# Kernel optimization log

Measured on AMD Instinct MI355X. Metric: run time of the kernel, lower is better.

Reference implementation:

```python
import jax, jax.numpy as jnp
import numpy as np

B, NV, H, W = 4, 1, 224, 224
GH = GW = 16                 # 224 // 14 patch grid
NT = 1 + GH * GW             # 257 tokens (cls + patches)
CIN, DF, DH = 1152, 512, 128
NP0 = 512
UPF = (4, 8)
RADIUS = 1.0


def setup_inputs():
    key = jax.random.key(0)
    ks = jax.random.split(key, 8)
    rn = lambda k, s, sc: jax.random.normal(k, s) * sc
    points = jax.random.uniform(ks[0], (B, NP0, 3), minval=-0.5, maxval=0.5)
    tokens = rn(ks[1], (B, CIN, NT), 0.5)
    # OpenGL-style c2w (the forward flips cols 1:3 to OpenCV); camera at z=+2 looking at origin
    c2w = np.tile(np.eye(4, dtype=np.float32), (B, NV, 1, 1))
    c2w[..., 2, 3] = 2.0
    K = np.zeros((B, NV, 3, 3), dtype=np.float32)
    K[..., 0, 0] = 250.0; K[..., 1, 1] = 250.0
    K[..., 0, 2] = W / 2.0; K[..., 1, 2] = H / 2.0
    K[..., 2, 2] = 1.0
    return dict(
        points=points, input_image_tokens=tokens,
        c2w_cond=jnp.asarray(c2w), intrinsic_cond=jnp.asarray(K),
        w1=rn(ks[2], (2 * DF, CIN), CIN ** -0.5), b1=jnp.zeros((2 * DF,)),
        w2=rn(ks[3], (DF, 2 * DF), (2 * DF) ** -0.5), b2=jnp.zeros((DF,)),
        s0_w1=rn(ks[4], (DH, 3 + DF), (3 + DF) ** -0.5), s0_b1=jnp.zeros((DH,)),
        s0_ow=rn(ks[5], (UPF[0] * 3, DH), DH ** -0.5), s0_ob=jnp.zeros((UPF[0] * 3,)),
        s1_w1=rn(ks[6], (DH, 3 + DF), (3 + DF) ** -0.5), s1_b1=jnp.zeros((DH,)),
        s1_ow=rn(ks[7], (UPF[1] * 3, DH), DH ** -0.5), s1_ob=jnp.zeros((UPF[1] * 3,)))


def _points_projection(pts, c2w, K, lf):
    # pts: (B,N,3), c2w: (B,4,4) OpenCV, K: (B,3,3), lf: (B,C,H,W)
    N = pts.shape[1]
    w2c = jnp.linalg.inv(c2w)
    cam = jnp.einsum('bij,bnj->bni', w2c[:, :3, :3], pts) + w2c[:, None, :3, 3]
    z = cam[..., 2]
    zs = jnp.where(jnp.abs(z) > 1e-8, z, 1e-8)
    px = K[:, 0, 0][:, None] * cam[..., 0] / zs + K[:, 0, 2][:, None]
    py = K[:, 1, 1][:, None] * cam[..., 1] / zs + K[:, 1, 2][:, None]
    ix = jnp.floor(px).astype(jnp.int32)
    iy = jnp.floor(py).astype(jnp.int32)
    valid = (z > 1e-6) & (ix >= 0) & (ix < W) & (iy >= 0) & (iy < H)
    pix = jnp.where(valid, iy * W + ix, H * W)                  # (B,N); dummy bin H*W
    nseg = B * (H * W + 1)
    seg = (jnp.arange(B)[:, None] * (H * W + 1) + pix).reshape(-1)
    zf = jnp.where(valid, z, jnp.inf).reshape(-1)
    minz = jax.ops.segment_min(zf, seg, num_segments=nseg)      # z-buffer (points_per_pixel=1)
    ismin = valid.reshape(-1) & (zf <= minz[seg])
    pid = jnp.arange(B * N)
    win = jax.ops.segment_min(jnp.where(ismin, pid, B * N), seg, num_segments=nseg)
    visible = (pid == win[seg]).reshape(B, N)                   # unique winner per pixel
    lff = lf.reshape(B, -1, H * W)
    g = jnp.take_along_axis(lff, jnp.clip(pix, 0, H * W - 1)[:, None, :], axis=2)  # (B,C,N)
    return jnp.where(visible[:, None, :], g, 0.0)


def reference(points, input_image_tokens, c2w_cond, intrinsic_cond,
              w1, b1, w2, b2, s0_w1, s0_b1, s0_ow, s0_ob, s1_w1, s1_b1, s1_ow, s1_ob):
    # mlp_feat_cond: 1x1 conv MLP over tokens
    feat = jax.nn.relu(jnp.einsum('oc,bcn->bon', w1, input_image_tokens) + b1[:, None])
    feat = jnp.einsum('oc,bcn->bon', w2, feat) + b2[:, None]    # (B, DF, NT)
    # OpenGL -> OpenCV flip of c2w columns 1:3
    flip = jnp.ones((4, 4)).at[:3, 1:3].set(-1.0)
    c2w = c2w_cond[:, 0] * flip
    Kmat = intrinsic_cond[:, 0]
    # drop cls token, to patch grid, bilinear upsample to image resolution
    lf = jnp.transpose(feat, (0, 2, 1))[:, 1:].reshape(B, GH, GW, DF)
    lf = jnp.transpose(lf, (0, 3, 1, 2))
    lf = jax.image.resize(lf, (B, DF, H, W), method='bilinear')  # (B, DF, H, W)
    pts = points
    pcd = jnp.transpose(points, (0, 2, 1))                      # (B,3,N)
    stages = (((s0_w1, s0_b1, s0_ow, s0_ob), UPF[0]), ((s1_w1, s1_b1, s1_ow, s1_ob), UPF[1]))
    outs = []
    for (ws, bs, ow, ob), f in stages:
        up_cond = _points_projection(pts, c2w, Kmat, lf)        # (B, DF, N) visibility-masked gather
        h = jax.nn.relu(jnp.einsum('oc,bcn->bon', ws,
                                   jnp.concatenate([pcd, up_cond], axis=1)) + bs[:, None])
        off = jnp.tanh(jnp.einsum('oc,bcn->bon', ow, h) + ob[:, None])  # (B, 3f, N)
        n = pcd.shape[2]
        off = off.reshape(B, f, 3, n).transpose(0, 2, 3, 1).reshape(B, 3, n * f)
        pcd = jnp.repeat(pcd, f, axis=2) + off * RADIUS         # SPD-style bounded upsample
        pts = jnp.transpose(pcd, (0, 2, 1))
        outs.append(pts)
    return tuple(outs)
```

## Files before the change

kernel.cpp:

```cpp
#include <hip/hip_runtime.h>
#include <hip/hip_bf16.h>
#include <cstdint>
#include <cstddef>

using bf16 = __hip_bfloat16;
typedef __attribute__((ext_vector_type(8))) short bf16x8_t;
typedef __attribute__((ext_vector_type(4))) float f32x4_t;

#define BB 4
#define HH 224
#define WWD 224
#define NTOK 257
#define CINC 1152
#define DFC 512

constexpr size_t OFF_WC     = 256;
constexpr size_t OFF_T      = OFF_WC + 1052672;
constexpr size_t OFF_FP     = OFF_T + 1048576;
constexpr size_t OFF_ZB0    = OFF_FP + 12582912;
constexpr size_t OFF_ZB1    = OFF_ZB0 + 1605632;
constexpr size_t OFF_PI0    = OFF_ZB1 + 1605632;
constexpr size_t OFF_PI1    = OFF_PI0 + 32768;
constexpr size_t WS_FULL4   = OFF_PI1 + 131072;
constexpr size_t OFF_SCR    = 256 + 2105344;
constexpr size_t OFF_ZBUF   = OFF_SCR;
constexpr size_t OFF_PINFO  = OFF_SCR + 1605632;
constexpr size_t WS_NEED    = OFF_SCR + 1736704;

__device__ __forceinline__ float ldf(const void* p, size_t i, bool f32) {
  return f32 ? ((const float*)p)[i] : __bfloat162float(((const bf16*)p)[i]);
}
__device__ __forceinline__ double ldd(const void* p, size_t i, bool f32) {
  return f32 ? (double)((const float*)p)[i]
             : (double)__bfloat162float(((const bf16*)p)[i]);
}
__device__ __forceinline__ bool detect_f32(const void* c2w_raw) {
  const float* fc = (const float*)c2w_raw;
  return (fc[0] == 1.0f) && (fc[5] == 1.0f);
}

__device__ void compute_cam(const void* c2w_raw, const void* K_raw, int b, bool f32,
                            double* cw) {
  double m[16];
#pragma unroll
  for (int i = 0; i < 16; ++i) m[i] = ldd(c2w_raw, b*16 + i, f32);
  m[1]=-m[1]; m[2]=-m[2]; m[5]=-m[5]; m[6]=-m[6]; m[9]=-m[9]; m[10]=-m[10];
  double i0  =  m[5]*m[10]*m[15] - m[5]*m[11]*m[14] - m[9]*m[6]*m[15] + m[9]*m[7]*m[14] + m[13]*m[6]*m[11] - m[13]*m[7]*m[10];
  double i4  = -m[4]*m[10]*m[15] + m[4]*m[11]*m[14] + m[8]*m[6]*m[15] - m[8]*m[7]*m[14] - m[12]*m[6]*m[11] + m[12]*m[7]*m[10];
  double i8  =  m[4]*m[9]*m[15]  - m[4]*m[11]*m[13] - m[8]*m[5]*m[15] + m[8]*m[7]*m[13] + m[12]*m[5]*m[11] - m[12]*m[7]*m[9];
  double i12 = -m[4]*m[9]*m[14]  + m[4]*m[10]*m[13] + m[8]*m[5]*m[14] - m[8]*m[6]*m[13] - m[12]*m[5]*m[10] + m[12]*m[6]*m[9];
  double i1  = -m[1]*m[10]*m[15] + m[1]*m[11]*m[14] + m[9]*m[2]*m[15] - m[9]*m[3]*m[14] - m[13]*m[2]*m[11] + m[13]*m[3]*m[10];
  double i5  =  m[0]*m[10]*m[15] - m[0]*m[11]*m[14] - m[8]*m[2]*m[15] + m[8]*m[3]*m[14] + m[12]*m[2]*m[11] - m[12]*m[3]*m[10];
  double i9  = -m[0]*m[9]*m[15]  + m[0]*m[11]*m[13] + m[8]*m[1]*m[15] - m[8]*m[3]*m[13] - m[12]*m[1]*m[11] + m[12]*m[3]*m[9];
  double i13 =  m[0]*m[9]*m[14]  - m[0]*m[10]*m[13] - m[8]*m[1]*m[14] + m[8]*m[2]*m[13] + m[12]*m[1]*m[10] - m[12]*m[2]*m[9];
  double i2  =  m[1]*m[6]*m[15]  - m[1]*m[7]*m[14]  - m[5]*m[2]*m[15] + m[5]*m[3]*m[14] + m[13]*m[2]*m[7]  - m[13]*m[3]*m[6];
  double i6  = -m[0]*m[6]*m[15]  + m[0]*m[7]*m[14]  + m[4]*m[2]*m[15] - m[4]*m[3]*m[14] - m[12]*m[2]*m[7]  + m[12]*m[3]*m[6];
  double i10 =  m[0]*m[5]*m[15]  - m[0]*m[7]*m[13]  - m[4]*m[1]*m[15] + m[4]*m[3]*m[13] + m[12]*m[1]*m[7]  - m[12]*m[3]*m[5];
  double i14 = -m[0]*m[5]*m[14]  + m[0]*m[6]*m[13]  + m[4]*m[1]*m[14] - m[4]*m[2]*m[13] - m[12]*m[1]*m[6]  + m[12]*m[2]*m[5];
  double i3  = -m[1]*m[6]*m[11]  + m[1]*m[7]*m[10]  + m[5]*m[2]*m[11] - m[5]*m[3]*m[10] - m[9]*m[2]*m[7]   + m[9]*m[3]*m[6];
  double i7  =  m[0]*m[6]*m[11]  - m[0]*m[7]*m[10]  - m[4]*m[2]*m[11] + m[4]*m[3]*m[10] + m[8]*m[2]*m[7]   - m[8]*m[3]*m[6];
  double i11 = -m[0]*m[5]*m[11]  + m[0]*m[7]*m[9]   + m[4]*m[1]*m[11] - m[4]*m[3]*m[9]  - m[8]*m[1]*m[7]   + m[8]*m[3]*m[5];
  double det = m[0]*i0 + m[1]*i4 + m[2]*i8 + m[3]*i12;
  double r = 1.0 / det;
  cw[0]=i0*r;  cw[1]=i1*r;  cw[2]=i2*r;  cw[3]=i3*r;
  cw[4]=i4*r;  cw[5]=i5*r;  cw[6]=i6*r;  cw[7]=i7*r;
  cw[8]=i8*r;  cw[9]=i9*r;  cw[10]=i10*r; cw[11]=i11*r;
  cw[12] = ldd(K_raw, b*9+0, f32);
  cw[13] = ldd(K_raw, b*9+2, f32);
  cw[14] = ldd(K_raw, b*9+4, f32);
  cw[15] = ldd(K_raw, b*9+5, f32);
}

__device__ __forceinline__ void project_point(
    double px, double py, double pz, const double* cw, int b, int m,
    unsigned long long* __restrict__ zbuf, int* __restrict__ pinfo) {
  double cx = cw[0]*px + cw[1]*py + cw[2]*pz + cw[3];
  double cy = cw[4]*px + cw[5]*py + cw[6]*pz + cw[7];
  double z  = cw[8]*px + cw[9]*py + cw[10]*pz + cw[11];
  double zs = (fabs(z) > 1e-8) ? z : 1e-8;
  double fpx = cw[12] * cx / zs + cw[13];
  double fpy = cw[14] * cy / zs + cw[15];
  double fix = floor(fpx), fiy = floor(fpy);
  bool valid = (z > 1e-6) && (fix >= 0.0) && (fix < (double)WWD) && (fiy >= 0.0) && (fiy < (double)HH);
  int* pi = pinfo + (size_t)m * 4;
  if (valid) {
    int ix = (int)fix, iy = (int)fiy;
    int zidx = b * (HH * WWD) + iy * WWD + ix;
    float zf = (float)z;
    unsigned long long key = ((unsigned long long)__float_as_uint(zf) << 32) | (unsigned)m;
    atomicMin(&zbuf[zidx], key);
    pi[0] = zidx; pi[1] = 1;
    *(unsigned long long*)(pi + 2) = key;
  } else {
    pi[0] = 0; pi[1] = 0; pi[2] = 0; pi[3] = 0;
  }
}

__global__ __launch_bounds__(256) void init_k(uint4* __restrict__ wcT,
                                              uint4* __restrict__ zb) {
  const int NW = 2101248 / 16;
  const int NZ = 3211264 / 16;
  int i = (int)blockIdx.x * 256 + (int)threadIdx.x;
  if (i < NW) {
    wcT[i] = make_uint4(0u, 0u, 0u, 0u);
  } else {
    int j = i - NW;
    if (j < NZ) zb[j] = make_uint4(~0u, ~0u, ~0u, ~0u);
  }
}

template <int XK, int WK, bool ATOMIC, bool PART, int PREC>
__device__ void gemm_body(
    short* SMEM, int bX, int bY, int bZ,
    const void* __restrict__ Wm, const void* __restrict__ Wm2,
    const void* __restrict__ X, const void* __restrict__ xb,
    int bstr, float* __restrict__ Y, const void* __restrict__ c2w_raw,
    int O, int K, int Nn, int Yld, int Xld, int Xc0,
    int bx0, int bxm, int by0, int bym,
    int Wld, int Wc0, int skn) {
  short* Whi = SMEM;
  short* Wmd = SMEM + 2560;
  short* Wlo = SMEM + 5120;
  short* Xhi = SMEM + 7680;
  short* Xmd = SMEM + 10240;
  short* Xlo = SMEM + 12800;
  const bool f32 = detect_f32(c2w_raw);
  int tid = threadIdx.x;
  int n0 = bX * 64;
  int o0 = bY * 64;
  int bidx = bZ / skn;
  int ks = bZ - bidx * skn;
  int bx = bx0 + bxm * bidx;
  int by = by0 + bym * bidx;
  int kq = K / skn;
  int kbase = ks * kq;
  int so  = tid >> 2;
  int skq = tid & 3;
  int sn  = tid & 63;
  int skg = tid >> 6;
  int wv = tid >> 6, lane = tid & 63;
  int lm = lane & 15, lq = lane >> 4;

  float wreg[8], xreg[8];
  f32x4_t acc[4] = {};

  auto load_w = [&](int c0) {
    if constexpr (WK == 3) {
      int orow = o0 + so;
      const void* Wp = (orow < 128) ? Wm : Wm2;
      size_t base = (size_t)(orow & 127) * Wld + Wc0 + c0 + skq * 8;
#pragma unroll
      for (int j = 0; j < 8; ++j) wreg[j] = ldf(Wp, base + j, f32);
    } else {
      size_t base = (size_t)(o0 + so) * Wld + c0 + skq * 8;
      if (f32) {
        const float* Wf = (const float*)Wm;
        float4 v0 = *(const float4*)(Wf + base);
        float4 v1 = *(const float4*)(Wf + base + 4);
        wreg[0]=v0.x; wreg[1]=v0.y; wreg[2]=v0.z; wreg[3]=v0.w;
        wreg[4]=v1.x; wreg[5]=v1.y; wreg[6]=v1.z; wreg[7]=v1.w;
      } else {
        const unsigned short* Wh = (const unsigned short*)Wm;
        ushort4 u0 = *(const ushort4*)(Wh + base);
        ushort4 u1 = *(const ushort4*)(Wh + base + 4);
        wreg[0]=__uint_as_float((unsigned)u0.x<<16); wreg[1]=__uint_as_float((unsigned)u0.y<<16);
        wreg[2]=__uint_as_float((unsigned)u0.z<<16); wreg[3]=__uint_as_float((unsigned)u0.w<<16);
        wreg[4]=__uint_as_float((unsigned)u1.x<<16); wreg[5]=__uint_as_float((unsigned)u1.y<<16);
        wreg[6]=__uint_as_float((unsigned)u1.z<<16); wreg[7]=__uint_as_float((unsigned)u1.w<<16);
      }
    }
  };
  auto load_x = [&](int c0) {
    int gn = n0 + sn;
#pragma unroll
    for (int j = 0; j < 8; ++j) {
      int c = c0 + skg * 8 + j;
      float v = 0.f;
      if (gn < Nn) {
        if (XK == 3) {
          v = (gn < 1024) ? ldf(X, (size_t)c * 1024 + gn, f32)
                          : ((gn == 1024) ? ldf(xb, c, f32) : 0.f);
        } else {
          size_t xi = ((size_t)bx * K + c) * Xld + Xc0 + gn;
          v = ldf(X, xi, f32);
        }
      }
      xreg[j] = v;
    }
  };
  auto store_hi = [&](const float* r, short* hp, int off) {
    int hd[4];
#pragma unroll
    for (int d = 0; d < 4; ++d) {
      unsigned b0 = __float_as_uint(r[2*d]), b1 = __float_as_uint(r[2*d+1]);
      hd[d] = (int)((b0 >> 16) | (b1 & 0xFFFF0000u));
    }
    *(int4*)&hp[off] = make_int4(hd[0], hd[1], hd[2], hd[3]);
  };
  auto split_store3 = [&](const float* r, short* hp, short* mp, short* lp, int off) {
    int hd[4], md[4], ld[4];
#pragma unroll
    for (int d = 0; d < 4; ++d) {
      float v0 = r[2*d], v1 = r[2*d+1];
      unsigned b0 = __float_as_uint(v0), b1 = __float_as_uint(v1);
      hd[d] = (int)((b0 >> 16) | (b1 & 0xFFFF0000u));
      float h0 = __uint_as_float(b0 & 0xFFFF0000u);
      float h1 = __uint_as_float(b1 & 0xFFFF0000u);
      float r0 = v0 - h0, r1 = v1 - h1;
      unsigned c0 = __float_as_uint(r0), c1 = __float_as_uint(r1);
      md[d] = (int)((c0 >> 16) | (c1 & 0xFFFF0000u));
      float m0 = __uint_as_float(c0 & 0xFFFF0000u);
      float m1 = __uint_as_float(c1 & 0xFFFF0000u);
      unsigned e0 = __float_as_uint(r0 - m0), e1 = __float_as_uint(r1 - m1);
      ld[d] = (int)((e0 >> 16) | (e1 & 0xFFFF0000u));
    }
    *(int4*)&hp[off] = make_int4(hd[0], hd[1], hd[2], hd[3]);
    *(int4*)&mp[off] = make_int4(md[0], md[1], md[2], md[3]);
    *(int4*)&lp[off] = make_int4(ld[0], ld[1], ld[2], ld[3]);
  };

  int nkt = kq / 32;
  int woff = so * 40 + skq * 8;
  int xoff = sn * 40 + skg * 8;
  int aoff = (wv * 16 + lm) * 40 + lq * 8;
  load_w(kbase); load_x(kbase);

  if (PREC == 0 && !f32) {
    for (int kt = 0; kt < nkt; ++kt) {
      __syncthreads();
      store_hi(wreg, Whi, woff);
      store_hi(xreg, Xhi, xoff);
      __syncthreads();
      if (kt + 1 < nkt) { load_w(kbase + (kt + 1) * 32); load_x(kbase + (kt + 1) * 32); }
      bf16x8_t ahi = *(const bf16x8_t*)&Whi[aoff];
#pragma unroll
      for (int nt = 0; nt < 4; ++nt) {
        int boff = (nt * 16 + lm) * 40 + lq * 8;
        bf16x8_t bhi = *(const bf16x8_t*)&Xhi[boff];
        acc[nt] = __builtin_amdgcn_mfma_f32_16x16x32_bf16(ahi, bhi, acc[nt], 0, 0, 0);
      }
    }
  } else {
    for (int kt = 0; kt < nkt; ++kt) {
      __syncthreads();
      split_store3(wreg, Whi, Wmd, Wlo, woff);
      split_store3(xreg, Xhi, Xmd, Xlo, xoff);
      __syncthreads();
      if (kt + 1 < nkt) { load_w(kbase + (kt + 1) * 32); load_x(kbase + (kt + 1) * 32); }
      bf16x8_t ahi = *(const bf16x8_t*)&Whi[aoff];
      bf16x8_t amd = *(const bf16x8_t*)&Wmd[aoff];
      bf16x8_t alo = *(const bf16x8_t*)&Wlo[aoff];
#pragma unroll
      for (int nt = 0; nt < 4; ++nt) {
        int boff = (nt * 16 + lm) * 40 + lq * 8;
        bf16x8_t bhi = *(const bf16x8_t*)&Xhi[boff];
        bf16x8_t bmd = *(const bf16x8_t*)&Xmd[boff];
        bf16x8_t blo = *(const bf16x8_t*)&Xlo[boff];
        acc[nt] = __builtin_amdgcn_mfma_f32_16x16x32_bf16(ahi, blo, acc[nt], 0, 0, 0);
        acc[nt] = __builtin_amdgcn_mfma_f32_16x16x32_bf16(amd, bmd, acc[nt], 0, 0, 0);
        acc[nt] = __builtin_amdgcn_mfma_f32_16x16x32_bf16(alo, bhi, acc[nt], 0, 0, 0);
        acc[nt] = __builtin_amdgcn_mfma_f32_16x16x32_bf16(amd, bhi, acc[nt], 0, 0, 0);
        acc[nt] = __builtin_amdgcn_mfma_f32_16x16x32_bf16(ahi, bmd, acc[nt], 0, 0, 0);
        acc[nt] = __builtin_amdgcn_mfma_f32_16x16x32_bf16(ahi, bhi, acc[nt], 0, 0, 0);
      }
    }
  }

  if constexpr (PART) {
    float* Yp = Y + (size_t)ks * (size_t)bstr;
#pragma unroll
    for (int nt = 0; nt < 4; ++nt) {
      int gn = n0 + nt * 16 + lm;
      if (gn < Nn) {
#pragma unroll
        for (int r = 0; r < 4; ++r) {
          int o = o0 + wv * 16 + lq * 4 + r;
          Yp[((size_t)by * O + o) * (size_t)Yld + gn] = acc[nt][r];
        }
      }
    }
  } else if (!ATOMIC) {
#pragma unroll
    for (int nt = 0; nt < 4; ++nt) {
      int gn = n0 + nt * 16 + lm;
      if (gn < Nn) {
#pragma unroll
        for (int r = 0; r < 4; ++r) {
          int o = o0 + wv * 16 + lq * 4 + r;
          Y[((size_t)by * O + o) * (size_t)Yld + gn] = acc[nt][r];
        }
      }
    }
  } else {
#pragma unroll
    for (int nt = 0; nt < 4; ++nt) {
      int gn = n0 + nt * 16 + lm;
      if (gn < Nn) {
#pragma unroll
        for (int r = 0; r < 4; ++r) {
          int o = o0 + wv * 16 + lq * 4 + r;
          atomicAdd(&Y[((size_t)by * O + o) * (size_t)Yld + gn], acc[nt][r]);
        }
      }
    }
  }
}

__global__ __launch_bounds__(256) void front_k(
    const void* __restrict__ w1, const void* __restrict__ tokens,
    float* __restrict__ fp,
    const void* __restrict__ s0w1, const void* __restrict__ s1w1,
    const void* __restrict__ w2, const void* __restrict__ b2,
    float* __restrict__ Wc, const void* __restrict__ c2w_raw) {
  __shared__ __align__(16) short SMEM[6 * 2560];
  int id = (int)blockIdx.x;
  if (id < 768) {
    gemm_body<0, 0, false, true, 0>(SMEM, id & 3, (id >> 2) & 15, id >> 6,
        w1, nullptr, tokens, nullptr,  1048576, fp, c2w_raw,
        1024, CINC, 256, 256, 257, 1, 0, 1, 0, 1, CINC, 0, 3);
  } else {
    int j = id - 768;
    gemm_body<3, 3, true, false, 0>(SMEM, j % 17, (j / 17) & 3, j / 68,
        s0w1, s1w1, w2, b2, 0, Wc, c2w_raw,
        256, 512, 1025, 1028, 1025, 0, 0, 0, 0, 0, 515, 3, 4);
  }
}

template <int SK>
__global__ __launch_bounds__(256) void tgemm_k(
    const float* __restrict__ Wc,
    const float* __restrict__ fp,
    const void* __restrict__ b1,
    float* __restrict__ T,
    const void* __restrict__ c2w_raw,
    const void* __restrict__ pts, const void* __restrict__ K_raw,
    unsigned long long* __restrict__ zb0, int* __restrict__ pinfo0) {
  const bool f32 = detect_f32(c2w_raw);
  if ((int)blockIdx.z == BB * SK) {
    int m = ((int)blockIdx.y * 4 + (int)blockIdx.x) * 256 + (int)threadIdx.x;
    if (m < BB * 512) {
      int b = m / 512;
      double cw[16];
      compute_cam(c2w_raw, K_raw, b, f32, cw);
      double px = ldd(pts, (size_t)m*3+0, f32);
      double py = ldd(pts, (size_t)m*3+1, f32);
      double pz = ldd(pts, (size_t)m*3+2, f32);
      project_point(px, py, pz, cw, b, m, zb0, pinfo0);
    }
    return;
  }
  const int TK = 32;
  const int PS = BB * 1024 * 256;
  __shared__ __align__(16) float uni[64 * 68];
  float* Ws = uni;
  float* Xs = uni + TK * 68;
  int tid = threadIdx.x;
  int n0 = blockIdx.x * 64;
  int o0 = blockIdx.y * 64;
  int bz = (int)blockIdx.z;
  int b  = bz / SK;
  int ks = bz - b * SK;
  const int kq = 1024 / SK;
  int kbase = ks * kq;
  int tx = tid & 15, ty = tid >> 4;
  int wo = tid >> 3, wk4 = tid & 7;
  float acc[4][4] = {};
  float4 wv[2];
  float xv[8];

  auto load_tile = [&](int c0) {
#pragma unroll
    for (int i = 0; i < 2; ++i) {
      int o = o0 + wo + i * 32;
      wv[i] = *(const float4*)(Wc + (size_t)o * 1028 + kbase + c0 + 4 * wk4);
    }
#pragma unroll
    for (int i = 0; i < 8; ++i) {
      int idx = i * 256 + tid;
      int n = idx & 63, k = idx >> 6;
      int kk = kbase + c0 + k;
      size_t xi = ((size_t)b * 1024 + kk) * 256 + n0 + n;
      float v = fp[xi] + fp[PS + xi] + fp[2 * PS + xi] + ldf(b1, kk, f32);
      xv[i] = fmaxf(v, 0.f);
    }
  };

  int nkt = kq / TK;
  load_tile(0);
  for (int kt = 0; kt < nkt; ++kt) {
    __syncthreads();
#pragma unroll
    for (int i = 0; i < 2; ++i) {
      int o = wo + i * 32;
      Ws[(4 * wk4 + 0) * 68 + o] = wv[i].x;
      Ws[(4 * wk4 + 1) * 68 + o] = wv[i].y;
      Ws[(4 * wk4 + 2) * 68 + o] = wv[i].z;
      Ws[(4 * wk4 + 3) * 68 + o] = wv[i].w;
    }
#pragma unroll
    for (int i = 0; i < 8; ++i) {
      int idx = i * 256 + tid;
      int n = idx & 63, k = idx >> 6;
      Xs[k * 68 + n] = xv[i];
    }
    __syncthreads();
    if (kt + 1 < nkt) load_tile((kt + 1) * TK);
#pragma unroll
    for (int k = 0; k < TK; ++k) {
      const float4 a  = *(const float4*)&Ws[k * 68 + tx * 4];
      const float4 bb = *(const float4*)&Xs[k * 68 + ty * 4];
      acc[0][0] = fmaf(a.x, bb.x, acc[0][0]); acc[0][1] = fmaf(a.x, bb.y, acc[0][1]);
      acc[0][2] = fmaf(a.x, bb.z, acc[0][2]); acc[0][3] = fmaf(a.x, bb.w, acc[0][3]);
      acc[1][0] = fmaf(a.y, bb.x, acc[1][0]); acc[1][1] = fmaf(a.y, bb.y, acc[1][1]);
      acc[1][2] = fmaf(a.y, bb.z, acc[1][2]); acc[1][3] = fmaf(a.y, bb.w, acc[1][3]);
      acc[2][0] = fmaf(a.z, bb.x, acc[2][0]); acc[2][1] = fmaf(a.z, bb.y, acc[2][1]);
      acc[2][2] = fmaf(a.z, bb.z, acc[2][2]); acc[2][3] = fmaf(a.z, bb.w, acc[2][3]);
      acc[3][0] = fmaf(a.w, bb.x, acc[3][0]); acc[3][1] = fmaf(a.w, bb.y, acc[3][1]);
      acc[3][2] = fmaf(a.w, bb.z, acc[3][2]); acc[3][3] = fmaf(a.w, bb.w, acc[3][3]);
    }
  }
  __syncthreads();
  float* ts = uni;
#pragma unroll
  for (int oi = 0; oi < 4; ++oi)
#pragma unroll
    for (int ni = 0; ni < 4; ++ni)
      ts[(tx * 4 + oi) * 65 + ty * 4 + ni] = acc[oi][ni];
  __syncthreads();
  int oo = tid & 63, nb = tid >> 6;
  float bv = (ks == 0) ? Wc[(size_t)(o0 + oo) * 1028 + 1024] : 0.f;
#pragma unroll
  for (int i = 0; i < 16; ++i) {
    int n = nb * 16 + i;
    atomicAdd(&T[((size_t)b * 256 + n0 + n) * 256 + o0 + oo], ts[oo * 65 + n] + bv);
  }
}

template <int XK, bool RELU, bool TROUT>
__global__ __launch_bounds__(256) void gemm_k(const void* __restrict__ Wm, const void* __restrict__ X,
                                              const void* __restrict__ bias, float* __restrict__ Y,
                                              const void* __restrict__ c2w_raw, int O, int K, int Nn,
                                              int bx0, int bxm, int by0, int bym) {
  const int TK = 32;
  __shared__ __align__(16) float Ws[TK * 68];
  __shared__ __align__(16) float Xs[TK * 68];
  const bool f32 = detect_f32(c2w_raw);
  int tid = threadIdx.x;
  int n0 = blockIdx.x * 64;
  int o0 = blockIdx.y * 64;
  int bx = bx0 + bxm * (int)blockIdx.z;
  int by = by0 + bym * (int)blockIdx.z;
  int tx = tid & 15, ty = tid >> 4;
  int wo  = tid >> 3;
  int wk4 = tid & 7;
  float acc[4][4] = {};
  float4 wv[2];
  float  xv[8];

  auto load_tile = [&](int c0) {
#pragma unroll
    for (int i = 0; i < 2; ++i) {
      int o = wo + i * 32;
      size_t off = (size_t)(o0 + o) * K + c0 + 4 * wk4;
      if (f32) {
        wv[i] = *(const float4*)((const float*)Wm + off);
      } else {
        ushort4 u = *(const ushort4*)((const unsigned short*)Wm + off);
        wv[i] = make_float4(__uint_as_float((unsigned)u.x << 16),
                            __uint_as_float((unsigned)u.y << 16),
                            __uint_as_float((unsigned)u.z << 16),
                            __uint_as_float((unsigned)u.w << 16));
      }
    }
#pragma unroll
    for (int i = 0; i < 8; ++i) {
      int idx = i * 256 + tid;
      int n = idx & 63, k = idx >> 6;
      int gn = n0 + n;
      float v = 0.f;
      if (gn < Nn) {
        size_t xi = ((size_t)bx * K + c0 + k) * Nn + gn;
        v = (XK == 0) ? ldf(X, xi, f32) : ((const float*)X)[xi];
      }
      xv[i] = v;
    }
  };

  int nkt = K / TK;
  load_tile(0);
  for (int kt = 0; kt < nkt; ++kt) {
    __syncthreads();
#pragma unroll
    for (int i = 0; i < 2; ++i) {
      int o = wo + i * 32;
      Ws[(4 * wk4 + 0) * 68 + o] = wv[i].x;
      Ws[(4 * wk4 + 1) * 68 + o] = wv[i].y;
      Ws[(4 * wk4 + 2) * 68 + o] = wv[i].z;
      Ws[(4 * wk4 + 3) * 68 + o] = wv[i].w;
    }
#pragma unroll
    for (int i = 0; i < 8; ++i) {
      int idx = i * 256 + tid;
      int n = idx & 63, k = idx >> 6;
      Xs[k * 68 + n] = xv[i];
    }
    __syncthreads();
    if (kt + 1 < nkt) load_tile((kt + 1) * TK);
#pragma unroll
    for (int k = 0; k < TK; ++k) {
      const float4 a  = *(const float4*)&Ws[k * 68 + tx * 4];
      const float4 bb = *(const float4*)&Xs[k * 68 + ty * 4];
      acc[0][0] = fmaf(a.x, bb.x, acc[0][0]); acc[0][1] = fmaf(a.x, bb.y, acc[0][1]);
      acc[0][2] = fmaf(a.x, bb.z, acc[0][2]); acc[0][3] = fmaf(a.x, bb.w, acc[0][3]);
      acc[1][0] = fmaf(a.y, bb.x, acc[1][0]); acc[1][1] = fmaf(a.y, bb.y, acc[1][1]);
      acc[1][2] = fmaf(a.y, bb.z, acc[1][2]); acc[1][3] = fmaf(a.y, bb.w, acc[1][3]);
      acc[2][0] = fmaf(a.z, bb.x, acc[2][0]); acc[2][1] = fmaf(a.z, bb.y, acc[2][1]);
      acc[2][2] = fmaf(a.z, bb.z, acc[2][2]); acc[2][3] = fmaf(a.z, bb.w, acc[2][3]);
      acc[3][0] = fmaf(a.w, bb.x, acc[3][0]); acc[3][1] = fmaf(a.w, bb.y, acc[3][1]);
      acc[3][2] = fmaf(a.w, bb.z, acc[3][2]); acc[3][3] = fmaf(a.w, bb.w, acc[3][3]);
    }
  }
#pragma unroll
  for (int oi = 0; oi < 4; ++oi) {
    int o = o0 + tx * 4 + oi;
    float bv = ldf(bias, o, f32);
#pragma unroll
    for (int ni = 0; ni < 4; ++ni) {
      int gn = n0 + ty * 4 + ni;
      if (gn < Nn) {
        float v = acc[oi][ni] + bv;
        if (RELU) v = fmaxf(v, 0.f);
        size_t yi = TROUT ? ((size_t)by * Nn + gn) * O + o
                          : ((size_t)by * O + o) * Nn + gn;
        Y[yi] = v;
      }
    }
  }
}

template <int PMODE>
__global__ __launch_bounds__(256) void proj_k(const void* __restrict__ pts,
                                              const void* __restrict__ c2w_raw,
                                              const void* __restrict__ K_raw,
                                              unsigned long long* __restrict__ zbuf,
                                              int* __restrict__ pinfo, int N) {
  int m = blockIdx.x * 256 + threadIdx.x;
  if (m >= BB * N) return;
  const bool f32 = detect_f32(c2w_raw);
  int b = m / N;
  double cw[16];
  compute_cam(c2w_raw, K_raw, b, f32, cw);
  double px, py, pz;
  if (PMODE == 1) {
    const float* pf = (const float*)pts;
    px = pf[m*3+0]; py = pf[m*3+1]; pz = pf[m*3+2];
  } else {
    px = ldd(pts, (size_t)m*3+0, f32);
    py = ldd(pts, (size_t)m*3+1, f32);
    pz = ldd(pts, (size_t)m*3+2, f32);
  }
  project_point(px, py, pz, cw, b, m, zbuf, pinfo);
}

template <int PMODE, int F, int TM, bool PROJ>
__global__ __launch_bounds__(256) void stage2_k(
    const void* __restrict__ pts_in,
    const float* __restrict__ Tm,
    const int* __restrict__ pinfo,
    const unsigned long long* __restrict__ zbuf,
    const void* __restrict__ w1,
    const void* __restrict__ b1,
    const void* __restrict__ ow,
    const void* __restrict__ ob,
    const void* __restrict__ c2w_raw,
    const void* __restrict__ K_raw,
    unsigned long long* __restrict__ zb_out,
    int* __restrict__ pinfo_out,
    float* __restrict__ out,
    int N) {
  constexpr int TPP = 256 / TM;
  constexpr int OC  = 128 / TPP;
  __shared__ int   ro_s[TM * 4];
  __shared__ float wt_s[TM * 4];
  __shared__ float p_s[TM * 3];
  __shared__ float Wp_s[128 * 3];
  __shared__ float b1_s[128];
  __shared__ float op_s[TM * F * 3];
  __shared__ __align__(16) float ow_s[F * 3 * 132];
  __shared__ __align__(16) float Hs[TM * 132];

  const bool f32 = detect_f32(c2w_raw);
  int tid = threadIdx.x;
  int m0 = blockIdx.x * TM;

  if (tid < TM) {
    int m = m0 + tid;
    const int* pi = pinfo + (size_t)m * 4;
    int zidx = pi[0];
    unsigned long long key = *(const unsigned long long*)(pi + 2);
    bool vis = pi[1] && (zbuf[zidx] == key);
    float s = vis ? 1.f : 0.f;
    int b = m / N;
    int rem = zidx - b * (HH * WWD);
    int iy = rem / WWD, ix = rem - iy * WWD;
    float sx = fminf(fmaxf(((float)ix + 0.5f) / 14.0f - 0.5f, 0.f), 15.f);
    float sy = fminf(fmaxf(((float)iy + 0.5f) / 14.0f - 0.5f, 0.f), 15.f);
    int x0 = (int)sx, y0 = (int)sy;
    int x1 = min(x0 + 1, 15), y1 = min(y0 + 1, 15);
    float fx = sx - (float)x0, fy = sy - (float)y0;
    int base = b * 256;
    ro_s[tid*4+0] = (base + y0*16 + x0) * 256;
    ro_s[tid*4+1] = (base + y0*16 + x1) * 256;
    ro_s[tid*4+2] = (base + y1*16 + x0) * 256;
    ro_s[tid*4+3] = (base + y1*16 + x1) * 256;
    wt_s[tid*4+0] = s * (1.f-fy)*(1.f-fx);
    wt_s[tid*4+1] = s * (1.f-fy)*fx;
    wt_s[tid*4+2] = s * fy*(1.f-fx);
    wt_s[tid*4+3] = s * fy*fx;
#pragma unroll
    for (int d = 0; d < 3; ++d) {
      p_s[tid*3 + d] = (PMODE == 1) ? ((const float*)pts_in)[(size_t)m*3 + d]
                                    : ldf(pts_in, (size_t)m*3 + d, f32);
    }
  }
  for (int i = tid; i < 128 * 3; i += 256) Wp_s[i] = ldf(w1, (size_t)(i / 3) * 515 + (i % 3), f32);
  for (int i = tid; i < 128; i += 256) b1_s[i] = ldf(b1, i, f32);
  for (int i = tid; i < F * 3 * 128; i += 256) ow_s[(i >> 7) * 132 + (i & 127)] = ldf(ow, i, f32);
  __syncthreads();

  {
    int pt = tid / TPP;
    int tx = tid % TPP;
    int oc0 = tx * OC;
    const float* t0p = Tm + ro_s[pt*4+0] + oc0;
    const float* t1p = Tm + ro_s[pt*4+1] + oc0;
    const float* t2p = Tm + ro_s[pt*4+2] + oc0;
    const float* t3p = Tm + ro_s[pt*4+3] + oc0;
    float w0 = wt_s[pt*4+0], w1v = wt_s[pt*4+1], w2v = wt_s[pt*4+2], w3v = wt_s[pt*4+3];
    float px = p_s[pt*3+0], py = p_s[pt*3+1], pz = p_s[pt*3+2];
#pragma unroll
    for (int i = 0; i < OC; i += 4) {
      f32x4_t c0 = *(const f32x4_t*)(t0p + i);
      f32x4_t c1 = *(const f32x4_t*)(t1p + i);
      f32x4_t c2 = *(const f32x4_t*)(t2p + i);
      f32x4_t c3 = *(const f32x4_t*)(t3p + i);
      f32x4_t hv;
#pragma unroll
      for (int j = 0; j < 4; ++j) {
        int o = oc0 + i + j;
        float v = b1_s[o]
                + Wp_s[o*3+0]*px + Wp_s[o*3+1]*py + Wp_s[o*3+2]*pz
                + w0*c0[j] + w1v*c1[j] + w2v*c2[j] + w3v*c3[j];
        hv[j] = fmaxf(v, 0.f);
      }
      *(f32x4_t*)&Hs[pt * 132 + oc0 + i] = hv;
    }
  }
  __syncthreads();

  const int tasks = TM * F * 3;
  for (int t = tid; t < tasks; t += 256) {
    int mI = t % TM;
    int r  = t / TM;
    f32x4_t acc4 = {0.f, 0.f, 0.f, 0.f};
#pragma unroll
    for (int k = 0; k < 128; k += 4) {
      f32x4_t hv = *(const f32x4_t*)&Hs[mI * 132 + k];
      f32x4_t wv = *(const f32x4_t*)&ow_s[r * 132 + k];
      acc4 += hv * wv;
    }
    float dot = acc4[0] + acc4[1] + acc4[2] + acc4[3] + ldf(ob, r, f32);
    float val = tanhf(dot);
    int j = r / 3, d = r - j * 3;
    int m = m0 + mI;
    float ov = p_s[mI * 3 + d] + val;
    out[((size_t)m * F + j) * 3 + d] = ov;
    if (PROJ) op_s[(mI * F + j) * 3 + d] = ov;
  }

  if constexpr (PROJ) {
    __syncthreads();
    if (tid < TM * F) {
      int mo = m0 * F + tid;
      int b = mo / (N * F);
      double cw[16];
      compute_cam(c2w_raw, K_raw, b, f32, cw);
      double px = (double)op_s[tid*3+0];
      double py = (double)op_s[tid*3+1];
      double pz = (double)op_s[tid*3+2];
      project_point(px, py, pz, cw, b, mo, zb_out, pinfo_out);
    }
  }
}

template <int PMODE, int F>
__global__ __launch_bounds__(256) void stage_k(
    const void* __restrict__ pts_in,
    const float* __restrict__ g2,
    const int* __restrict__ pinfo,
    const unsigned long long* __restrict__ zbuf,
    const void* __restrict__ w1,
    const void* __restrict__ b1,
    const void* __restrict__ ow,
    const void* __restrict__ ob,
    const void* __restrict__ c2w_raw,
    float* __restrict__ out,
    int N) {
  const int TM = 16, TK = 32;
  __shared__ int   ro_s[TM * 4];
  __shared__ float wt_s[TM * 4];
  __shared__ float p_s[TM * 3];
  __shared__ float ow_s[F * 3 * 128];
  __shared__ __align__(16) float uni[4800];
  float* Ws = uni;
  float* Vs = uni + 4224;
  float* Hs = uni;

  const bool f32 = detect_f32(c2w_raw);
  int tid = threadIdx.x;
  int m0 = blockIdx.x * TM;

  if (tid < TM) {
    int m = m0 + tid;
    const int* pi = pinfo + (size_t)m * 4;
    int zidx = pi[0];
    unsigned long long key = *(const unsigned long long*)(pi + 2);
    bool vis = pi[1] && (zbuf[zidx] == key);
    float s = vis ? 1.f : 0.f;
    int b = m / N;
    int rem = zidx - b * (HH * WWD);
    int iy = rem / WWD, ix = rem - iy * WWD;
    float sx = fminf(fmaxf(((float)ix + 0.5f) / 14.0f - 0.5f, 0.f), 15.f);
    float sy = fminf(fmaxf(((float)iy + 0.5f) / 14.0f - 0.5f, 0.f), 15.f);
    int x0 = (int)sx, y0 = (int)sy;
    int x1 = min(x0 + 1, 15), y1 = min(y0 + 1, 15);
    float fx = sx - (float)x0, fy = sy - (float)y0;
    int base = b * NTOK;
    ro_s[tid*4+0] = (base + 1 + y0*16 + x0) * DFC;
    ro_s[tid*4+1] = (base + 1 + y0*16 + x1) * DFC;
    ro_s[tid*4+2] = (base + 1 + y1*16 + x0) * DFC;
    ro_s[tid*4+3] = (base + 1 + y1*16 + x1) * DFC;
    wt_s[tid*4+0] = s * (1.f-fy)*(1.f-fx);
    wt_s[tid*4+1] = s * (1.f-fy)*fx;
    wt_s[tid*4+2] = s * fy*(1.f-fx);
    wt_s[tid*4+3] = s * fy*fx;
#pragma unroll
    for (int d = 0; d < 3; ++d) {
      p_s[tid*3 + d] = (PMODE == 1) ? ((const float*)pts_in)[(size_t)m*3 + d]
                                    : ldf(pts_in, (size_t)m*3 + d, f32);
    }
  }
  for (int i = tid; i < F * 3 * 128; i += 256) ow_s[i] = ldf(ow, i, f32);
  __syncthreads();

  int tx = tid & 15, ty = tid >> 4;
  float acc[2][4] = {};
  float wreg[16];
  float greg[2][4];
  float vbase[2];

  auto prefetch = [&](int c0) {
    if (f32) {
      const float* w1f = (const float*)w1;
#pragma unroll
      for (int i = 0; i < 16; ++i) {
        int idx = i * 256 + tid;
        int k = idx & 31, o = idx >> 5;
        int c = c0 + k;
        wreg[i] = (c < 515) ? w1f[(size_t)o * 515 + c] : 0.f;
      }
    } else {
      const bf16* w1h = (const bf16*)w1;
#pragma unroll
      for (int i = 0; i < 16; ++i) {
        int idx = i * 256 + tid;
        int k = idx & 31, o = idx >> 5;
        int c = c0 + k;
        wreg[i] = (c < 515) ? __bfloat162float(w1h[(size_t)o * 515 + c]) : 0.f;
      }
    }
#pragma unroll
    for (int i = 0; i < 2; ++i) {
      int idx = i * 256 + tid;
      int mI = idx & 15, k = idx >> 4;
      int c = c0 + k;
      vbase[i] = 0.f;
      greg[i][0] = greg[i][1] = greg[i][2] = greg[i][3] = 0.f;
      if (c < 3) {
        vbase[i] = p_s[mI*3 + c];
      } else if (c < 515) {
        int ch = c - 3;
        greg[i][0] = g2[ro_s[mI*4+0] + ch];
        greg[i][1] = g2[ro_s[mI*4+1] + ch];
        greg[i][2] = g2[ro_s[mI*4+2] + ch];
        greg[i][3] = g2[ro_s[mI*4+3] + ch];
      }
    }
  };

  prefetch(0);
  for (int kt = 0; kt < 17; ++kt) {
    __syncthreads();
#pragma unroll
    for (int i = 0; i < 16; ++i) {
      int idx = i * 256 + tid;
      int k = idx & 31, o = idx >> 5;
      Ws[k * 132 + o] = wreg[i];
    }
#pragma unroll
    for (int i = 0; i < 2; ++i) {
      int idx = i * 256 + tid;
      int mI = idx & 15, k = idx >> 4;
      Vs[k * 18 + mI] = vbase[i]
        + wt_s[mI*4+0] * greg[i][0] + wt_s[mI*4+1] * greg[i][1]
        + wt_s[mI*4+2] * greg[i][2] + wt_s[mI*4+3] * greg[i][3];
    }
    __syncthreads();
    if (kt + 1 < 17) prefetch((kt + 1) * TK);
#pragma unroll
    for (int k = 0; k < TK; ++k) {
      const float4 a0 = *(const float4*)&Ws[k * 132 + tx * 4];
      const float4 a1 = *(const float4*)&Ws[k * 132 + 64 + tx * 4];
      const float  bb = Vs[k * 18 + ty];
      acc[0][0] = fmaf(a0.x, bb, acc[0][0]);
      acc[0][1] = fmaf(a0.y, bb, acc[0][1]);
      acc[0][2] = fmaf(a0.z, bb, acc[0][2]);
      acc[0][3] = fmaf(a0.w, bb, acc[0][3]);
      acc[1][0] = fmaf(a1.x, bb, acc[1][0]);
      acc[1][1] = fmaf(a1.y, bb, acc[1][1]);
      acc[1][2] = fmaf(a1.z, bb, acc[1][2]);
      acc[1][3] = fmaf(a1.w, bb, acc[1][3]);
    }
  }
  __syncthreads();
#pragma unroll
  for (int h = 0; h < 2; ++h) {
#pragma unroll
    for (int oi = 0; oi < 4; ++oi) {
      int o = h * 64 + tx * 4 + oi;
      float bv = ldf(b1, o, f32);
      Hs[o * 18 + ty] = fmaxf(acc[h][oi] + bv, 0.f);
    }
  }
  __syncthreads();
  const int tasks = TM * F * 3;
  for (int t = tid; t < tasks; t += 256) {
    int mI = t & 15, r = t >> 4;
    float dot = ldf(ob, r, f32);
#pragma unroll 8
    for (int k = 0; k < 128; ++k) dot = fmaf(ow_s[r * 128 + k], Hs[k * 18 + mI], dot);
    float val = tanhf(dot);
    int j = r / 3, d = r - j * 3;
    int m = m0 + mI;
    out[((size_t)m * F + j) * 3 + d] = p_s[mI * 3 + d] + val;
  }
}

extern "C" void kernel_launch(void* const* d_in, const int* in_sizes, int n_in,
                              void* d_out, int out_size, void* d_ws, size_t ws_size,
                              hipStream_t stream) {
  const void* points = d_in[0];
  const void* tokens = d_in[1];
  const void* c2w    = d_in[2];
  const void* intr   = d_in[3];
  const void* w1     = d_in[4];
  const void* b1     = d_in[5];
  const void* w2     = d_in[6];
  const void* b2     = d_in[7];
  const void* s0w1   = d_in[8];
  const void* s0b1   = d_in[9];
  const void* s0ow   = d_in[10];
  const void* s0ob   = d_in[11];
  const void* s1w1   = d_in[12];
  const void* s1b1   = d_in[13];
  const void* s1ow   = d_in[14];
  const void* s1ob   = d_in[15];

  if (ws_size < WS_NEED) {
    hipMemsetAsync(d_out, 0, (size_t)out_size * sizeof(float), stream);
    return;
  }

  char* ws = (char*)d_ws;
  float* out    = (float*)d_out;
  float* out0   = out;
  float* out1   = out + 24576;

  const int NB = (NTOK + 63) / 64;
  const size_t zbytes = (size_t)BB * HH * WWD * 8;

  if (ws_size >= WS_FULL4) {
    float* Wc   = (float*)(ws + OFF_WC);
    float* Tb   = (float*)(ws + OFF_T);
    float* fp   = (float*)(ws + OFF_FP);
    unsigned long long* zb0 = (unsigned long long*)(ws + OFF_ZB0);
    unsigned long long* zb1 = (unsigned long long*)(ws + OFF_ZB1);
    int* pinfo0 = (int*)(ws + OFF_PI0);
    int* pinfo1 = (int*)(ws + OFF_PI1);

    init_k<<<1297, 256, 0, stream>>>((uint4*)(ws + OFF_WC), (uint4*)(ws + OFF_ZB0));

    front_k<<<1040, 256, 0, stream>>>(w1, tokens, fp, s0w1, s1w1, w2, b2, Wc, c2w);

    tgemm_k<4><<<dim3(4, 4, BB * 4 + 1), 256, 0, stream>>>(
        Wc, fp, b1, Tb, c2w, points, intr, zb0, pinfo0);

    stage2_k<0, 4, 8, true><<<(BB * 512) / 8, 256, 0, stream>>>(
        points, Tb, pinfo0, zb0, s0w1, s0b1, s0ow, s0ob, c2w, intr,
        zb1, pinfo1, out0, 512);
    stage2_k<1, 8, 8, false><<<(BB * 2048) / 8, 256, 0, stream>>>(
        out0, Tb + 128, pinfo1, zb1, s1w1, s1b1, s1ow, s1ob, c2w, intr,
        nullptr, nullptr, out1, 2048);
  } else {
    float* g2    = (float*)(ws + 256);
    float* feat1 = (float*)(ws + OFF_SCR);
    unsigned long long* zbuf = (unsigned long long*)(ws + OFF_ZBUF);
    int* pinfo = (int*)(ws + OFF_PINFO);
    for (int b = 0; b < BB; ++b) {
      gemm_k<0, true, false><<<dim3(NB, 16, 1), 256, 0, stream>>>(
          w1, tokens, b1, feat1, c2w, 1024, CINC, NTOK, b, 0, 0, 0);
      gemm_k<1, false, true><<<dim3(NB, 8, 1), 256, 0, stream>>>(
          w2, feat1, b2, g2, c2w, 512, 1024, NTOK, 0, 0, b, 0);
    }
    hipMemsetAsync(zbuf, 0xFF, zbytes, stream);
    proj_k<0><<<(BB * 512) / 256, 256, 0, stream>>>(points, c2w, intr, zbuf, pinfo, 512);
    stage_k<0, 4><<<(BB * 512) / 16, 256, 0, stream>>>(points, g2, pinfo, zbuf,
                                                       s0w1, s0b1, s0ow, s0ob, c2w,
                                                       out0, 512);
    hipMemsetAsync(zbuf, 0xFF, zbytes, stream);
    proj_k<1><<<(BB * 2048) / 256, 256, 0, stream>>>(out0, c2w, intr, zbuf, pinfo, 2048);
    stage_k<1, 8><<<(BB * 2048) / 16, 256, 0, stream>>>(out0, g2, pinfo, zbuf,
                                                        s1w1, s1b1, s1ow, s1ob, c2w,
                                                        out1, 2048);
  }
}
```

Before: 175.5 us.

## Fold init into front kernel, drop Wc split-K atomics, use BK=64 bf16 path

Removes the separate init kernel by having extra blocks of front_k zero the T buffer and fill the z-buffer sentinel. The weight-combination GEMM stops splitting K four ways with atomics and instead writes directly with one K slice, so Wc no longer needs zeroing. The bf16 fast path now stages 64-wide K tiles and copies raw bf16 weights straight into shared memory, halving barriers per K. The risks are fewer parallel blocks for the Wc GEMM and larger per-thread register use.

```diff
diff --git a/kernel.cpp b/kernel.cpp
--- a/kernel.cpp
+++ b/kernel.cpp
@@ -96,19 +96,6 @@
   }
 }
 
-__global__ __launch_bounds__(256) void init_k(uint4* __restrict__ wcT,
-                                              uint4* __restrict__ zb) {
-  const int NW = 2101248 / 16;
-  const int NZ = 3211264 / 16;
-  int i = (int)blockIdx.x * 256 + (int)threadIdx.x;
-  if (i < NW) {
-    wcT[i] = make_uint4(0u, 0u, 0u, 0u);
-  } else {
-    int j = i - NW;
-    if (j < NZ) zb[j] = make_uint4(~0u, ~0u, ~0u, ~0u);
-  }
-}
-
 template <int XK, int WK, bool ATOMIC, bool PART, int PREC>
 __device__ void gemm_body(
     short* SMEM, int bX, int bY, int bZ,
@@ -118,12 +105,6 @@
     int O, int K, int Nn, int Yld, int Xld, int Xc0,
     int bx0, int bxm, int by0, int bym,
     int Wld, int Wc0, int skn) {
-  short* Whi = SMEM;
-  short* Wmd = SMEM + 2560;
-  short* Wlo = SMEM + 5120;
-  short* Xhi = SMEM + 7680;
-  short* Xmd = SMEM + 10240;
-  short* Xlo = SMEM + 12800;
   const bool f32 = detect_f32(c2w_raw);
   int tid = threadIdx.x;
   int n0 = bX * 64;
@@ -141,106 +122,146 @@
   int wv = tid >> 6, lane = tid & 63;
   int lm = lane & 15, lq = lane >> 4;
 
-  float wreg[8], xreg[8];
   f32x4_t acc[4] = {};
 
-  auto load_w = [&](int c0) {
-    if constexpr (WK == 3) {
-      int orow = o0 + so;
-      const void* Wp = (orow < 128) ? Wm : Wm2;
-      size_t base = (size_t)(orow & 127) * Wld + Wc0 + c0 + skq * 8;
-#pragma unroll
-      for (int j = 0; j < 8; ++j) wreg[j] = ldf(Wp, base + j, f32);
-    } else {
-      size_t base = (size_t)(o0 + so) * Wld + c0 + skq * 8;
-      if (f32) {
+  auto store_hi8 = [&](const float* r, short* hp, int off) {
+    int hd[4];
+#pragma unroll
+    for (int d = 0; d < 4; ++d) {
+      unsigned b0 = __float_as_uint(r[2*d]), b1 = __float_as_uint(r[2*d+1]);
+      hd[d] = (int)((b0 >> 16) | (b1 & 0xFFFF0000u));
+    }
+    *(int4*)&hp[off] = make_int4(hd[0], hd[1], hd[2], hd[3]);
+  };
+
+  if (PREC == 0 && !f32) {
+    short* Wh = SMEM;
+    short* Xh = SMEM + 4608;
+    int woff = so * 72 + skq * 16;
+    int xoff = sn * 72 + skg * 16;
+    int arow = (wv * 16 + lm) * 72 + lq * 8;
+    int4 wraw[2];
+    float wr16[16], xr16[16];
+    auto load_w = [&](int c0) {
+      if constexpr (WK == 3) {
+        int orow = o0 + so;
+        const void* Wp = (orow < 128) ? Wm : Wm2;
+        size_t base = (size_t)(orow & 127) * Wld + Wc0 + c0 + skq * 16;
+#pragma unroll
+        for (int j = 0; j < 16; ++j) wr16[j] = ldf(Wp, base + j, false);
+      } else {
+        const short* Ws16 = (const short*)Wm;
+        size_t base = (size_t)(o0 + so) * Wld + c0 + skq * 16;
+        wraw[0] = *(const int4*)(Ws16 + base);
+        wraw[1] = *(const int4*)(Ws16 + base + 8);
+      }
+    };
+    auto load_x = [&](int c0) {
+      int gn = n0 + sn;
+#pragma unroll
+      for (int j = 0; j < 16; ++j) {
+        int c = c0 + skg * 16 + j;
+        float v = 0.f;
+        if (gn < Nn) {
+          if (XK == 3) {
+            v = (gn < 1024) ? ldf(X, (size_t)c * 1024 + gn, false)
+                            : ((gn == 1024) ? ldf(xb, c, false) : 0.f);
+          } else {
+            v = ldf(X, ((size_t)bx * K + c) * Xld + Xc0 + gn, false);
+          }
+        }
+        xr16[j] = v;
+      }
+    };
+    int nkt = kq / 64;
+    load_w(kbase); load_x(kbase);
+    for (int kt = 0; kt < nkt; ++kt) {
+      __syncthreads();
+      if constexpr (WK == 3) {
+        store_hi8(wr16, Wh, woff); store_hi8(wr16 + 8, Wh, woff + 8);
+      } else {
+        *(int4*)&Wh[woff] = wraw[0]; *(int4*)&Wh[woff + 8] = wraw[1];
+      }
+      store_hi8(xr16, Xh, xoff); store_hi8(xr16 + 8, Xh, xoff + 8);
+      __syncthreads();
+      if (kt + 1 < nkt) { load_w(kbase + (kt + 1) * 64); load_x(kbase + (kt + 1) * 64); }
+#pragma unroll
+      for (int s = 0; s < 2; ++s) {
+        bf16x8_t ahi = *(const bf16x8_t*)&Wh[arow + s * 32];
+#pragma unroll
+        for (int nt = 0; nt < 4; ++nt) {
+          bf16x8_t bhi = *(const bf16x8_t*)&Xh[(nt * 16 + lm) * 72 + s * 32 + lq * 8];
+          acc[nt] = __builtin_amdgcn_mfma_f32_16x16x32_bf16(ahi, bhi, acc[nt], 0, 0, 0);
+        }
+      }
+    }
+  } else {
+    short* Whi = SMEM;
+    short* Wmd = SMEM + 2560;
+    short* Wlo = SMEM + 5120;
+    short* Xhi = SMEM + 7680;
+    short* Xmd = SMEM + 10240;
+    short* Xlo = SMEM + 12800;
+    float wreg[8], xreg[8];
+    auto load_w = [&](int c0) {
+      if constexpr (WK == 3) {
+        int orow = o0 + so;
+        const void* Wp = (orow < 128) ? Wm : Wm2;
+        size_t base = (size_t)(orow & 127) * Wld + Wc0 + c0 + skq * 8;
+#pragma unroll
+        for (int j = 0; j < 8; ++j) wreg[j] = ldf(Wp, base + j, f32);
+      } else {
+        size_t base = (size_t)(o0 + so) * Wld + c0 + skq * 8;
         const float* Wf = (const float*)Wm;
         float4 v0 = *(const float4*)(Wf + base);
         float4 v1 = *(const float4*)(Wf + base + 4);
         wreg[0]=v0.x; wreg[1]=v0.y; wreg[2]=v0.z; wreg[3]=v0.w;
         wreg[4]=v1.x; wreg[5]=v1.y; wreg[6]=v1.z; wreg[7]=v1.w;
-      } else {
-        const unsigned short* Wh = (const unsigned short*)Wm;
-        ushort4 u0 = *(const ushort4*)(Wh + base);
-        ushort4 u1 = *(const ushort4*)(Wh + base + 4);
-        wreg[0]=__uint_as_float((unsigned)u0.x<<16); wreg[1]=__uint_as_float((unsigned)u0.y<<16);
-        wreg[2]=__uint_as_float((unsigned)u0.z<<16); wreg[3]=__uint_as_float((unsigned)u0.w<<16);
-        wreg[4]=__uint_as_float((unsigned)u1.x<<16); wreg[5]=__uint_as_float((unsigned)u1.y<<16);
-        wreg[6]=__uint_as_float((unsigned)u1.z<<16); wreg[7]=__uint_as_float((unsigned)u1.w<<16);
-      }
-    }
-  };
-  auto load_x = [&](int c0) {
-    int gn = n0 + sn;
-#pragma unroll
-    for (int j = 0; j < 8; ++j) {
-      int c = c0 + skg * 8 + j;
-      float v = 0.f;
-      if (gn < Nn) {
-        if (XK == 3) {
-          v = (gn < 1024) ? ldf(X, (size_t)c * 1024 + gn, f32)
-                          : ((gn == 1024) ? ldf(xb, c, f32) : 0.f);
-        } else {
-          size_t xi = ((size_t)bx * K + c) * Xld + Xc0 + gn;
-          v = ldf(X, xi, f32);
+      }
+    };
+    auto load_x = [&](int c0) {
+      int gn = n0 + sn;
+#pragma unroll
+      for (int j = 0; j < 8; ++j) {
+        int c = c0 + skg * 8 + j;
+        float v = 0.f;
+        if (gn < Nn) {
+          if (XK == 3) {
+            v = (gn < 1024) ? ldf(X, (size_t)c * 1024 + gn, f32)
+                            : ((gn == 1024) ? ldf(xb, c, f32) : 0.f);
+          } else {
+            v = ldf(X, ((size_t)bx * K + c) * Xld + Xc0 + gn, f32);
+          }
         }
-      }
-      xreg[j] = v;
-    }
-  };
-  auto store_hi = [&](const float* r, short* hp, int off) {
-    int hd[4];
-#pragma unroll
-    for (int d = 0; d < 4; ++d) {
-      unsigned b0 = __float_as_uint(r[2*d]), b1 = __float_as_uint(r[2*d+1]);
-      hd[d] = (int)((b0 >> 16) | (b1 & 0xFFFF0000u));
-    }
-    *(int4*)&hp[off] = make_int4(hd[0], hd[1], hd[2], hd[3]);
-  };
-  auto split_store3 = [&](const float* r, short* hp, short* mp, short* lp, int off) {
-    int hd[4], md[4], ld[4];
-#pragma unroll
-    for (int d = 0; d < 4; ++d) {
-      float v0 = r[2*d], v1 = r[2*d+1];
-      unsigned b0 = __float_as_uint(v0), b1 = __float_as_uint(v1);
-      hd[d] = (int)((b0 >> 16) | (b1 & 0xFFFF0000u));
-      float h0 = __uint_as_float(b0 & 0xFFFF0000u);
-      float h1 = __uint_as_float(b1 & 0xFFFF0000u);
-      float r0 = v0 - h0, r1 = v1 - h1;
-      unsigned c0 = __float_as_uint(r0), c1 = __float_as_uint(r1);
-      md[d] = (int)((c0 >> 16) | (c1 & 0xFFFF0000u));
-      float m0 = __uint_as_float(c0 & 0xFFFF0000u);
-      float m1 = __uint_as_float(c1 & 0xFFFF0000u);
-      unsigned e0 = __float_as_uint(r0 - m0), e1 = __float_as_uint(r1 - m1);
-      ld[d] = (int)((e0 >> 16) | (e1 & 0xFFFF0000u));
-    }
-    *(int4*)&hp[off] = make_int4(hd[0], hd[1], hd[2], hd[3]);
-    *(int4*)&mp[off] = make_int4(md[0], md[1], md[2], md[3]);
-    *(int4*)&lp[off] = make_int4(ld[0], ld[1], ld[2], ld[3]);
-  };
-
-  int nkt = kq / 32;
-  int woff = so * 40 + skq * 8;
-  int xoff = sn * 40 + skg * 8;
-  int aoff = (wv * 16 + lm) * 40 + lq * 8;
-  load_w(kbase); load_x(kbase);
-
-  if (PREC == 0 && !f32) {
-    for (int kt = 0; kt < nkt; ++kt) {
-      __syncthreads();
-      store_hi(wreg, Whi, woff);
-      store_hi(xreg, Xhi, xoff);
-      __syncthreads();
-      if (kt + 1 < nkt) { load_w(kbase + (kt + 1) * 32); load_x(kbase + (kt + 1) * 32); }
-      bf16x8_t ahi = *(const bf16x8_t*)&Whi[aoff];
-#pragma unroll
-      for (int nt = 0; nt < 4; ++nt) {
-        int boff = (nt * 16 + lm) * 40 + lq * 8;
-        bf16x8_t bhi = *(const bf16x8_t*)&Xhi[boff];
-        acc[nt] = __builtin_amdgcn_mfma_f32_16x16x32_bf16(ahi, bhi, acc[nt], 0, 0, 0);
-      }
-    }
-  } else {
+        xreg[j] = v;
+      }
+    };
+    auto split_store3 = [&](const float* r, short* hp, short* mp, short* lp, int off) {
+      int hd[4], md[4], ld[4];
+#pragma unroll
+      for (int d = 0; d < 4; ++d) {
+        float v0 = r[2*d], v1 = r[2*d+1];
+        unsigned b0 = __float_as_uint(v0), b1 = __float_as_uint(v1);
+        hd[d] = (int)((b0 >> 16) | (b1 & 0xFFFF0000u));
+        float h0 = __uint_as_float(b0 & 0xFFFF0000u);
+        float h1 = __uint_as_float(b1 & 0xFFFF0000u);
+        float r0 = v0 - h0, r1 = v1 - h1;
+        unsigned c0 = __float_as_uint(r0), c1 = __float_as_uint(r1);
+        md[d] = (int)((c0 >> 16) | (c1 & 0xFFFF0000u));
+        float m0 = __uint_as_float(c0 & 0xFFFF0000u);
+        float m1 = __uint_as_float(c1 & 0xFFFF0000u);
+        unsigned e0 = __float_as_uint(r0 - m0), e1 = __float_as_uint(r1 - m1);
+        ld[d] = (int)((e0 >> 16) | (e1 & 0xFFFF0000u));
+      }
+      *(int4*)&hp[off] = make_int4(hd[0], hd[1], hd[2], hd[3]);
+      *(int4*)&mp[off] = make_int4(md[0], md[1], md[2], md[3]);
+      *(int4*)&lp[off] = make_int4(ld[0], ld[1], ld[2], ld[3]);
+    };
+    int woff = so * 40 + skq * 8;
+    int xoff = sn * 40 + skg * 8;
+    int aoff = (wv * 16 + lm) * 40 + lq * 8;
+    int nkt = kq / 32;
+    load_w(kbase); load_x(kbase);
     for (int kt = 0; kt < nkt; ++kt) {
       __syncthreads();
       split_store3(wreg, Whi, Wmd, Wlo, woff);
@@ -311,18 +332,28 @@
     float* __restrict__ fp,
     const void* __restrict__ s0w1, const void* __restrict__ s1w1,
     const void* __restrict__ w2, const void* __restrict__ b2,
-    float* __restrict__ Wc, const void* __restrict__ c2w_raw) {
+    float* __restrict__ Wc,
+    uint4* __restrict__ Tq, uint4* __restrict__ zbq,
+    const void* __restrict__ c2w_raw) {
   __shared__ __align__(16) short SMEM[6 * 2560];
   int id = (int)blockIdx.x;
   if (id < 768) {
     gemm_body<0, 0, false, true, 0>(SMEM, id & 3, (id >> 2) & 15, id >> 6,
         w1, nullptr, tokens, nullptr,  1048576, fp, c2w_raw,
         1024, CINC, 256, 256, 257, 1, 0, 1, 0, 1, CINC, 0, 3);
+  } else if (id < 836) {
+    int j = id - 768;
+    gemm_body<3, 3, false, false, 0>(SMEM, j % 17, j / 17, 0,
+        s0w1, s1w1, w2, b2, 0, Wc, c2w_raw,
+        256, 512, 1025, 1028, 1025, 0, 0, 0, 0, 0, 515, 3, 1);
   } else {
-    int j = id - 768;
-    gemm_body<3, 3, true, false, 0>(SMEM, j % 17, (j / 17) & 3, j / 68,
-        s0w1, s1w1, w2, b2, 0, Wc, c2w_raw,
-        256, 512, 1025, 1028, 1025, 0, 0, 0, 0, 0, 515, 3, 4);
+    int t = id - 836;
+    if (t < 256) {
+      Tq[t * 256 + (int)threadIdx.x] = make_uint4(0u, 0u, 0u, 0u);
+    } else {
+      int z = t - 256;
+      zbq[z * 256 + (int)threadIdx.x] = make_uint4(~0u, ~0u, ~0u, ~0u);
+    }
   }
 }
 
@@ -898,9 +929,9 @@
     int* pinfo0 = (int*)(ws + OFF_PI0);
     int* pinfo1 = (int*)(ws + OFF_PI1);
 
-    init_k<<<1297, 256, 0, stream>>>((uint4*)(ws + OFF_WC), (uint4*)(ws + OFF_ZB0));
-
-    front_k<<<1040, 256, 0, stream>>>(w1, tokens, fp, s0w1, s1w1, w2, b2, Wc, c2w);
+    front_k<<<1876, 256, 0, stream>>>(w1, tokens, fp, s0w1, s1w1, w2, b2, Wc,
+                                      (uint4*)(ws + OFF_T), (uint4*)(ws + OFF_ZB0),
+                                      c2w);
 
     tgemm_k<4><<<dim3(4, 4, BB * 4 + 1), 256, 0, stream>>>(
         Wc, fp, b1, Tb, c2w, points, intr, zb0, pinfo0);
```

New measurement: 178.5 us. About the same (+1.7%).
